# Kernel optimization log

Hardware: AMD Instinct MI355X
Metric: run time of the kernel (lower is better)

The kernel has to match this reference:

```python
import jax, jax.numpy as jnp
import numpy as np

N = 8192       # nodes
E = 262144     # edges (avg degree 32)
F_IN, H, L = 512, 256, 64


def setup_inputs() -> dict:
    key = jax.random.key(0)
    ks = jax.random.split(key, 8)
    features = jax.random.normal(ks[0], (N, F_IN), dtype=jnp.float32)
    src = jax.random.randint(ks[1], (E,), 0, N)
    dst = jax.random.randint(ks[2], (E,), 0, N)
    # nn.Linear weights are [out_feats, in_feats]; scale ~ kaiming-ish small init
    W1 = jax.random.normal(ks[3], (H, F_IN), dtype=jnp.float32) * (1.0 / np.sqrt(F_IN))
    b1 = jnp.zeros((H,), dtype=jnp.float32)
    W2 = jax.random.normal(ks[4], (L, H), dtype=jnp.float32) * (1.0 / np.sqrt(H))
    b2 = jnp.zeros((L,), dtype=jnp.float32)
    W3 = jax.random.normal(ks[5], (L, H), dtype=jnp.float32) * (1.0 / np.sqrt(H))
    b3 = jnp.zeros((L,), dtype=jnp.float32)
    return {"features": features, "src": src, "dst": dst,
            "W1": W1, "b1": b1, "W2": W2, "b2": b2, "W3": W3, "b3": b3}


def _gcn_agg(h, src, dst):
    # DGL copy_src + sum: gather source node features along edges, scatter-sum to dst
    return jax.ops.segment_sum(h[src], dst, num_segments=N)  # [N, d]


def reference(features, src, dst, W1, b1, W2, b2, W3, b3):
    # GCN layer 1: aggregate then linear + relu  (dropout=0 -> identity)
    agg1 = _gcn_agg(features, src, dst)                 # [N, F_IN]
    hidden = jax.nn.relu(agg1 @ W1.T + b1)              # [N, H]
    # GCN layers 2 & 3 share the aggregated hidden (linear activation)
    agg2 = _gcn_agg(hidden, src, dst)                   # [N, H]
    mu = agg2 @ W2.T + b2                               # [N, L]
    logvar = agg2 @ W3.T + b3                           # [N, L]
    # eval-mode reparameterize: z = mu
    z = mu
    # inner-product decoder with sigmoid
    adj = jax.nn.sigmoid(z @ z.T)                       # [N, N]
    return adj, mu, logvar
```

## Files before the change

kernel.cpp:

```cpp
#include <hip/hip_runtime.h>
#include <hip/hip_bf16.h>
#include <type_traits>

#define N_NODES 8192
#define N_EDGES 262144

typedef __attribute__((ext_vector_type(8))) short short8v;
typedef __attribute__((ext_vector_type(4))) float float4v;

static __device__ __forceinline__ unsigned short f2bf(float f) {
    unsigned u = __float_as_uint(f);
    unsigned r = (u + 0x7FFF + ((u >> 16) & 1)) >> 16;
    return (unsigned short)r;
}
static __device__ __forceinline__ float bf2f(unsigned short h) {
    return __uint_as_float(((unsigned)h) << 16);
}


__global__ __launch_bounds__(256) void hist_kernel(const int* __restrict__ dst, int* __restrict__ deg) {
    int e = blockIdx.x * 256 + threadIdx.x;
    if (e < N_EDGES) atomicAdd(&deg[dst[e]], 1);
}

__global__ __launch_bounds__(1024) void scan_kernel(const int* __restrict__ deg, int* __restrict__ offs) {
    __shared__ int sums[1024];
    int t = threadIdx.x;
    int v[8];
    int s = 0;
#pragma unroll
    for (int i = 0; i < 8; i++) { v[i] = deg[t * 8 + i]; s += v[i]; }
    sums[t] = s;
    __syncthreads();
    for (int off = 1; off < 1024; off <<= 1) {
        int x = (t >= off) ? sums[t - off] : 0;
        __syncthreads();
        sums[t] += x;
        __syncthreads();
    }
    int ex = (t == 0) ? 0 : sums[t - 1];
#pragma unroll
    for (int i = 0; i < 8; i++) { offs[t * 8 + i] = ex; ex += v[i]; }
    if (t == 1023) offs[N_NODES] = ex;
}

__global__ __launch_bounds__(256) void scatter_kernel(const int* __restrict__ src, const int* __restrict__ dst,
                                                      const int* __restrict__ offs, int* __restrict__ cur,
                                                      int* __restrict__ csr) {
    int e = blockIdx.x * 256 + threadIdx.x;
    if (e < N_EDGES) {
        int d = dst[e];
        int p = atomicAdd(&cur[d], 1);
        csr[offs[d] + p] = src[e];
    }
}

__global__ __launch_bounds__(256) void concat_w_kernel(const float* __restrict__ W2, const float* __restrict__ W3,
                                                       float* __restrict__ W23) {
    int i = blockIdx.x * 256 + threadIdx.x;
    if (i < 16384) W23[i] = W2[i];
    else if (i < 32768) W23[i] = W3[i - 16384];
}


template <int BM, int BN, int BK, int TM, int TN, bool BF16_OUT>
__global__ __launch_bounds__(256) void gemm_nt(const float* __restrict__ A, const float* __restrict__ B,
                                               void* __restrict__ Cv, int M, int N, int K) {
    __shared__ float As[BK][BM + 4];
    __shared__ float Bs[BK][BN + 4];
    const int tid = threadIdx.x;
    const int tc = tid % (BN / TN);
    const int tr = tid / (BN / TN);
    const int m0 = blockIdx.x * BM;
    const int n0 = blockIdx.y * BN;
    float acc[TM][TN] = {};
    for (int k0 = 0; k0 < K; k0 += BK) {
        constexpr int A_LOADS = BM * BK / (256 * 4);
#pragma unroll
        for (int i = 0; i < A_LOADS; i++) {
            int idx = (tid + i * 256) * 4;
            int am = idx / BK, ak = idx % BK;
            float4 v = *(const float4*)&A[(size_t)(m0 + am) * K + k0 + ak];
            As[ak + 0][am] = v.x; As[ak + 1][am] = v.y; As[ak + 2][am] = v.z; As[ak + 3][am] = v.w;
        }
        constexpr int B_LOADS = BN * BK / (256 * 4);
#pragma unroll
        for (int i = 0; i < B_LOADS; i++) {
            int idx = (tid + i * 256) * 4;
            int bn = idx / BK, bk = idx % BK;
            float4 v = *(const float4*)&B[(size_t)(n0 + bn) * K + k0 + bk];
            Bs[bk + 0][bn] = v.x; Bs[bk + 1][bn] = v.y; Bs[bk + 2][bn] = v.z; Bs[bk + 3][bn] = v.w;
        }
        __syncthreads();
#pragma unroll
        for (int k = 0; k < BK; k++) {
            float a[TM], b[TN];
#pragma unroll
            for (int i = 0; i < TM; i += 4) *(float4*)&a[i] = *(const float4*)&As[k][tr * TM + i];
#pragma unroll
            for (int j = 0; j < TN; j += 4) *(float4*)&b[j] = *(const float4*)&Bs[k][tc * TN + j];
#pragma unroll
            for (int i = 0; i < TM; i++)
#pragma unroll
                for (int j = 0; j < TN; j++) acc[i][j] = fmaf(a[i], b[j], acc[i][j]);
        }
        __syncthreads();
    }
#pragma unroll
    for (int i = 0; i < TM; i++) {
        size_t row = (size_t)(m0 + tr * TM + i) * N + n0 + tc * TN;
        if constexpr (BF16_OUT) {
            unsigned short* C = (unsigned short*)Cv;
#pragma unroll
            for (int j = 0; j < TN; j += 4) {
                ushort4 v;
                v.x = f2bf(acc[i][j]); v.y = f2bf(acc[i][j + 1]);
                v.z = f2bf(acc[i][j + 2]); v.w = f2bf(acc[i][j + 3]);
                *(ushort4*)&C[row + j] = v;
            }
        } else {
            float* C = (float*)Cv;
#pragma unroll
            for (int j = 0; j < TN; j += 4) {
                float4 v = {acc[i][j], acc[i][j + 1], acc[i][j + 2], acc[i][j + 3]};
                *(float4*)&C[row + j] = v;
            }
        }
    }
}


__global__ __launch_bounds__(256) void agg_relu_kernel(const unsigned short* __restrict__ Yb,
                                                       const int* __restrict__ offs,
                                                       const int* __restrict__ csr, const float* __restrict__ bias,
                                                       float* __restrict__ out) {
    int node = blockIdx.x * 4 + (threadIdx.x >> 6);
    int lane = threadIdx.x & 63;
    int s = offs[node], e = offs[node + 1];
    float4 acc = {0.f, 0.f, 0.f, 0.f};
    for (int i = s; i < e; i++) {
        int u = csr[i];
        ushort4 v = *(const ushort4*)&Yb[(size_t)u * 256 + lane * 4];
        acc.x += bf2f(v.x); acc.y += bf2f(v.y); acc.z += bf2f(v.z); acc.w += bf2f(v.w);
    }
    float4 b = *(const float4*)&bias[lane * 4];
    acc.x = fmaxf(acc.x + b.x, 0.f);
    acc.y = fmaxf(acc.y + b.y, 0.f);
    acc.z = fmaxf(acc.z + b.z, 0.f);
    acc.w = fmaxf(acc.w + b.w, 0.f);
    *(float4*)&out[(size_t)node * 256 + lane * 4] = acc;
}


__global__ __launch_bounds__(256) void agg_split_kernel(const unsigned short* __restrict__ Zb,
                                                        const int* __restrict__ offs,
                                                        const int* __restrict__ csr, const float* __restrict__ b2,
                                                        const float* __restrict__ b3, float* __restrict__ mu,
                                                        float* __restrict__ lv, unsigned short* __restrict__ zb) {
    int node = blockIdx.x * 4 + (threadIdx.x >> 6);
    int lane = threadIdx.x & 63;
    int s = offs[node], e = offs[node + 1];
    float2 acc = {0.f, 0.f};
    for (int i = s; i < e; i++) {
        int u = csr[i];
        ushort2 v = *(const ushort2*)&Zb[(size_t)u * 128 + lane * 2];
        acc.x += bf2f(v.x); acc.y += bf2f(v.y);
    }
    int col = lane * 2;
    if (col < 64) {
        acc.x += b2[col]; acc.y += b2[col + 1];
        *(float2*)&mu[(size_t)node * 64 + col] = acc;
        ushort2 q = {f2bf(acc.x), f2bf(acc.y)};
        *(ushort2*)&zb[(size_t)node * 64 + col] = q;
    } else {
        col -= 64;
        acc.x += b3[col]; acc.y += b3[col + 1];
        *(float2*)&lv[(size_t)node * 64 + col] = acc;
    }
}


__global__ __launch_bounds__(256) void adj_mfma_kernel(const unsigned short* __restrict__ zb,
                                                       float* __restrict__ out) {
    const int tid = threadIdx.x;
    const int lane = tid & 63;
    const int wid = tid >> 6;
    const int waveM = wid >> 1, waveN = wid & 1;
    const int m_base = blockIdx.x * 128 + waveM * 64;
    const int n_base = blockIdx.y * 128 + waveN * 64;
    const int r = lane & 15;
    const int q = lane >> 4;

    short8v a[4][2], b[4][2];
#pragma unroll
    for (int i = 0; i < 4; i++)
#pragma unroll
        for (int s = 0; s < 2; s++) {
            a[i][s] = *(const short8v*)&zb[(size_t)(m_base + i * 16 + r) * 64 + s * 32 + q * 8];
            b[i][s] = *(const short8v*)&zb[(size_t)(n_base + i * 16 + r) * 64 + s * 32 + q * 8];
        }

    float4v acc[4][4] = {};
#pragma unroll
    for (int s = 0; s < 2; s++)
#pragma unroll
        for (int i = 0; i < 4; i++)
#pragma unroll
            for (int j = 0; j < 4; j++)
                acc[i][j] = __builtin_amdgcn_mfma_f32_16x16x32_bf16(a[i][s], b[j][s], acc[i][j], 0, 0, 0);

#pragma unroll
    for (int i = 0; i < 4; i++)
#pragma unroll
        for (int j = 0; j < 4; j++) {
            int col = n_base + j * 16 + r;
#pragma unroll
            for (int t = 0; t < 4; t++) {
                int row = m_base + i * 16 + q * 4 + t;
                float v = 1.0f / (1.0f + __expf(-acc[i][j][t]));
                out[(size_t)row * N_NODES + col] = v;
            }
        }
}


extern "C" void kernel_launch(void* const* d_in, const int* in_sizes, int n_in,
                              void* d_out, int out_size, void* d_ws, size_t ws_size,
                              hipStream_t stream) {
    const float* X   = (const float*)d_in[0];
    const int*   src = (const int*)d_in[1];
    const int*   dst = (const int*)d_in[2];
    const float* W1  = (const float*)d_in[3];
    const float* b1  = (const float*)d_in[4];
    const float* W2  = (const float*)d_in[5];
    const float* b2  = (const float*)d_in[6];
    const float* W3  = (const float*)d_in[7];
    const float* b3  = (const float*)d_in[8];

    float* out    = (float*)d_out;
    float* adj    = out;
    float* mu_out = out + (size_t)N_NODES * N_NODES;
    float* lv_out = mu_out + (size_t)N_NODES * 64;

    char* ws = (char*)d_ws;
    int* deg             = (int*)(ws + 0);
    int* cur             = (int*)(ws + 32768);
    int* offs            = (int*)(ws + 65536);
    int* csr             = (int*)(ws + 98816);
    float* W23           = (float*)(ws + 1179648);
    unsigned short* Y1b  = (unsigned short*)(ws + 1310720);
    float* hidden        = (float*)(ws + 5505024);
    unsigned short* Zb   = (unsigned short*)(ws + 13893632);
    unsigned short* zb   = (unsigned short*)(ws + 15990784);

    hipMemsetAsync(deg, 0, 2 * N_NODES * sizeof(int), stream);
    hist_kernel<<<N_EDGES / 256, 256, 0, stream>>>(dst, deg);
    scan_kernel<<<1, 1024, 0, stream>>>(deg, offs);
    scatter_kernel<<<N_EDGES / 256, 256, 0, stream>>>(src, dst, offs, cur, csr);
    concat_w_kernel<<<128, 256, 0, stream>>>(W2, W3, W23);

    gemm_nt<64, 64, 16, 4, 4, true><<<dim3(128, 4), 256, 0, stream>>>(X, W1, Y1b, 8192, 256, 512);
    agg_relu_kernel<<<N_NODES / 4, 256, 0, stream>>>(Y1b, offs, csr, b1, hidden);
    gemm_nt<64, 64, 16, 4, 4, true><<<dim3(128, 2), 256, 0, stream>>>(hidden, W23, Zb, 8192, 128, 256);
    agg_split_kernel<<<N_NODES / 4, 256, 0, stream>>>(Zb, offs, csr, b2, b3, mu_out, lv_out, zb);
    adj_mfma_kernel<<<dim3(64, 64), 256, 0, stream>>>(zb, adj);
}
```

Baseline: 419.9 us.

## Switch dense GEMMs to bf16 MFMA with pre-cast inputs and bf16 hidden

```diff
diff --git a/kernel.cpp b/kernel.cpp
--- a/kernel.cpp
+++ b/kernel.cpp
@@ -1,6 +1,5 @@
 #include <hip/hip_runtime.h>
 #include <hip/hip_bf16.h>
-#include <type_traits>
 
 #define N_NODES 8192
 #define N_EDGES 262144
@@ -55,100 +54,97 @@
     }
 }
 
-__global__ __launch_bounds__(256) void concat_w_kernel(const float* __restrict__ W2, const float* __restrict__ W3,
-                                                       float* __restrict__ W23) {
-    int i = blockIdx.x * 256 + threadIdx.x;
-    if (i < 16384) W23[i] = W2[i];
-    else if (i < 32768) W23[i] = W3[i - 16384];
-}
-
-
-template <int BM, int BN, int BK, int TM, int TN, bool BF16_OUT>
-__global__ __launch_bounds__(256) void gemm_nt(const float* __restrict__ A, const float* __restrict__ B,
-                                               void* __restrict__ Cv, int M, int N, int K) {
-    __shared__ float As[BK][BM + 4];
-    __shared__ float Bs[BK][BN + 4];
+
+__global__ __launch_bounds__(256) void prep_cast_kernel(const float* __restrict__ X, const float* __restrict__ W1,
+                                                        const float* __restrict__ W2, const float* __restrict__ W3,
+                                                        unsigned short* __restrict__ Xb,
+                                                        unsigned short* __restrict__ W1b,
+                                                        unsigned short* __restrict__ W23b) {
+    int i4 = (blockIdx.x * 256 + threadIdx.x) * 4;
+    const float* srcp;
+    unsigned short* dstp;
+    int off;
+    if (i4 < 4194304)      { srcp = X;  dstp = Xb;           off = i4; }
+    else if (i4 < 4325376) { srcp = W1; dstp = W1b;          off = i4 - 4194304; }
+    else if (i4 < 4341760) { srcp = W2; dstp = W23b;         off = i4 - 4325376; }
+    else                   { srcp = W3; dstp = W23b + 16384; off = i4 - 4341760; }
+    float4 v = *(const float4*)&srcp[off];
+    ushort4 o = {f2bf(v.x), f2bf(v.y), f2bf(v.z), f2bf(v.w)};
+    *(ushort4*)&dstp[off] = o;
+}
+
+
+template <int MI, int NJ, int WN>
+__global__ __launch_bounds__(256) void gemm_nt_mfma(const unsigned short* __restrict__ A,
+                                                    const unsigned short* __restrict__ B,
+                                                    unsigned short* __restrict__ C,
+                                                    int N, int K) {
+    constexpr int MW = 4 / WN;
     const int tid = threadIdx.x;
-    const int tc = tid % (BN / TN);
-    const int tr = tid / (BN / TN);
-    const int m0 = blockIdx.x * BM;
-    const int n0 = blockIdx.y * BN;
-    float acc[TM][TN] = {};
-    for (int k0 = 0; k0 < K; k0 += BK) {
-        constexpr int A_LOADS = BM * BK / (256 * 4);
-#pragma unroll
-        for (int i = 0; i < A_LOADS; i++) {
-            int idx = (tid + i * 256) * 4;
-            int am = idx / BK, ak = idx % BK;
-            float4 v = *(const float4*)&A[(size_t)(m0 + am) * K + k0 + ak];
-            As[ak + 0][am] = v.x; As[ak + 1][am] = v.y; As[ak + 2][am] = v.z; As[ak + 3][am] = v.w;
-        }
-        constexpr int B_LOADS = BN * BK / (256 * 4);
-#pragma unroll
-        for (int i = 0; i < B_LOADS; i++) {
-            int idx = (tid + i * 256) * 4;
-            int bn = idx / BK, bk = idx % BK;
-            float4 v = *(const float4*)&B[(size_t)(n0 + bn) * K + k0 + bk];
-            Bs[bk + 0][bn] = v.x; Bs[bk + 1][bn] = v.y; Bs[bk + 2][bn] = v.z; Bs[bk + 3][bn] = v.w;
-        }
-        __syncthreads();
-#pragma unroll
-        for (int k = 0; k < BK; k++) {
-            float a[TM], b[TN];
-#pragma unroll
-            for (int i = 0; i < TM; i += 4) *(float4*)&a[i] = *(const float4*)&As[k][tr * TM + i];
-#pragma unroll
-            for (int j = 0; j < TN; j += 4) *(float4*)&b[j] = *(const float4*)&Bs[k][tc * TN + j];
-#pragma unroll
-            for (int i = 0; i < TM; i++)
-#pragma unroll
-                for (int j = 0; j < TN; j++) acc[i][j] = fmaf(a[i], b[j], acc[i][j]);
-        }
-        __syncthreads();
-    }
-#pragma unroll
-    for (int i = 0; i < TM; i++) {
-        size_t row = (size_t)(m0 + tr * TM + i) * N + n0 + tc * TN;
-        if constexpr (BF16_OUT) {
-            unsigned short* C = (unsigned short*)Cv;
-#pragma unroll
-            for (int j = 0; j < TN; j += 4) {
-                ushort4 v;
-                v.x = f2bf(acc[i][j]); v.y = f2bf(acc[i][j + 1]);
-                v.z = f2bf(acc[i][j + 2]); v.w = f2bf(acc[i][j + 3]);
-                *(ushort4*)&C[row + j] = v;
-            }
-        } else {
-            float* C = (float*)Cv;
-#pragma unroll
-            for (int j = 0; j < TN; j += 4) {
-                float4 v = {acc[i][j], acc[i][j + 1], acc[i][j + 2], acc[i][j + 3]};
-                *(float4*)&C[row + j] = v;
+    const int lane = tid & 63;
+    const int w = tid >> 6;
+    const int r = lane & 15, q = lane >> 4;
+    const int m0 = blockIdx.x * (MI * 16 * MW) + (w / WN) * (MI * 16);
+    const int n0 = blockIdx.y * (NJ * 16 * WN) + (w % WN) * (NJ * 16);
+    float4v acc[MI][NJ] = {};
+    for (int k = 0; k < K; k += 32) {
+        short8v a[MI], b[NJ];
+#pragma unroll
+        for (int i = 0; i < MI; i++)
+            a[i] = *(const short8v*)&A[(size_t)(m0 + i * 16 + r) * K + k + q * 8];
+#pragma unroll
+        for (int j = 0; j < NJ; j++)
+            b[j] = *(const short8v*)&B[(size_t)(n0 + j * 16 + r) * K + k + q * 8];
+#pragma unroll
+        for (int i = 0; i < MI; i++)
+#pragma unroll
+            for (int j = 0; j < NJ; j++)
+                acc[i][j] = __builtin_amdgcn_mfma_f32_16x16x32_bf16(a[i], b[j], acc[i][j], 0, 0, 0);
+    }
+#pragma unroll
+    for (int i = 0; i < MI; i++)
+#pragma unroll
+        for (int j = 0; j < NJ; j++) {
+            int col = n0 + j * 16 + r;
+#pragma unroll
+            for (int t = 0; t < 4; t++) {
+                int row = m0 + i * 16 + q * 4 + t;
+                C[(size_t)row * N + col] = f2bf(acc[i][j][t]);
             }
         }
-    }
 }
 
 
 __global__ __launch_bounds__(256) void agg_relu_kernel(const unsigned short* __restrict__ Yb,
                                                        const int* __restrict__ offs,
                                                        const int* __restrict__ csr, const float* __restrict__ bias,
-                                                       float* __restrict__ out) {
+                                                       unsigned short* __restrict__ out) {
     int node = blockIdx.x * 4 + (threadIdx.x >> 6);
     int lane = threadIdx.x & 63;
     int s = offs[node], e = offs[node + 1];
     float4 acc = {0.f, 0.f, 0.f, 0.f};
-    for (int i = s; i < e; i++) {
+    int i = s;
+    for (; i + 1 < e; i += 2) {
+        int u0 = csr[i], u1 = csr[i + 1];
+        ushort4 v0 = *(const ushort4*)&Yb[(size_t)u0 * 256 + lane * 4];
+        ushort4 v1 = *(const ushort4*)&Yb[(size_t)u1 * 256 + lane * 4];
+        acc.x += bf2f(v0.x) + bf2f(v1.x);
+        acc.y += bf2f(v0.y) + bf2f(v1.y);
+        acc.z += bf2f(v0.z) + bf2f(v1.z);
+        acc.w += bf2f(v0.w) + bf2f(v1.w);
+    }
+    if (i < e) {
         int u = csr[i];
         ushort4 v = *(const ushort4*)&Yb[(size_t)u * 256 + lane * 4];
         acc.x += bf2f(v.x); acc.y += bf2f(v.y); acc.z += bf2f(v.z); acc.w += bf2f(v.w);
     }
     float4 b = *(const float4*)&bias[lane * 4];
-    acc.x = fmaxf(acc.x + b.x, 0.f);
-    acc.y = fmaxf(acc.y + b.y, 0.f);
-    acc.z = fmaxf(acc.z + b.z, 0.f);
-    acc.w = fmaxf(acc.w + b.w, 0.f);
-    *(float4*)&out[(size_t)node * 256 + lane * 4] = acc;
+    ushort4 o;
+    o.x = f2bf(fmaxf(acc.x + b.x, 0.f));
+    o.y = f2bf(fmaxf(acc.y + b.y, 0.f));
+    o.z = f2bf(fmaxf(acc.z + b.z, 0.f));
+    o.w = f2bf(fmaxf(acc.w + b.w, 0.f));
+    *(ushort4*)&out[(size_t)node * 256 + lane * 4] = o;
 }
 
 
@@ -161,7 +157,15 @@
     int lane = threadIdx.x & 63;
     int s = offs[node], e = offs[node + 1];
     float2 acc = {0.f, 0.f};
-    for (int i = s; i < e; i++) {
+    int i = s;
+    for (; i + 1 < e; i += 2) {
+        int u0 = csr[i], u1 = csr[i + 1];
+        ushort2 v0 = *(const ushort2*)&Zb[(size_t)u0 * 128 + lane * 2];
+        ushort2 v1 = *(const ushort2*)&Zb[(size_t)u1 * 128 + lane * 2];
+        acc.x += bf2f(v0.x) + bf2f(v1.x);
+        acc.y += bf2f(v0.y) + bf2f(v1.y);
+    }
+    if (i < e) {
         int u = csr[i];
         ushort2 v = *(const ushort2*)&Zb[(size_t)u * 128 + lane * 2];
         acc.x += bf2f(v.x); acc.y += bf2f(v.y);
@@ -243,25 +247,33 @@
     float* lv_out = mu_out + (size_t)N_NODES * 64;
 
     char* ws = (char*)d_ws;
-    int* deg             = (int*)(ws + 0);
-    int* cur             = (int*)(ws + 32768);
-    int* offs            = (int*)(ws + 65536);
-    int* csr             = (int*)(ws + 98816);
-    float* W23           = (float*)(ws + 1179648);
-    unsigned short* Y1b  = (unsigned short*)(ws + 1310720);
-    float* hidden        = (float*)(ws + 5505024);
-    unsigned short* Zb   = (unsigned short*)(ws + 13893632);
-    unsigned short* zb   = (unsigned short*)(ws + 15990784);
+    size_t off = 0;
+    auto alloc = [&](size_t bytes) -> void* {
+        void* p = ws + off;
+        off += (bytes + 1023) & ~(size_t)1023;
+        return p;
+    };
+    int* deg            = (int*)alloc(N_NODES * 4);
+    int* cur            = (int*)alloc(N_NODES * 4);
+    int* offs           = (int*)alloc((N_NODES + 1) * 4);
+    int* csr            = (int*)alloc(N_EDGES * 4);
+    unsigned short* Xb  = (unsigned short*)alloc((size_t)N_NODES * 512 * 2);
+    unsigned short* W1b = (unsigned short*)alloc(256 * 512 * 2);
+    unsigned short* W23b= (unsigned short*)alloc(128 * 256 * 2);
+    unsigned short* Y1b = (unsigned short*)alloc((size_t)N_NODES * 256 * 2);
+    unsigned short* Hb  = (unsigned short*)alloc((size_t)N_NODES * 256 * 2);
+    unsigned short* Zb  = (unsigned short*)alloc((size_t)N_NODES * 128 * 2);
+    unsigned short* zb  = (unsigned short*)alloc((size_t)N_NODES * 64 * 2);
 
     hipMemsetAsync(deg, 0, 2 * N_NODES * sizeof(int), stream);
     hist_kernel<<<N_EDGES / 256, 256, 0, stream>>>(dst, deg);
     scan_kernel<<<1, 1024, 0, stream>>>(deg, offs);
     scatter_kernel<<<N_EDGES / 256, 256, 0, stream>>>(src, dst, offs, cur, csr);
-    concat_w_kernel<<<128, 256, 0, stream>>>(W2, W3, W23);
-
-    gemm_nt<64, 64, 16, 4, 4, true><<<dim3(128, 4), 256, 0, stream>>>(X, W1, Y1b, 8192, 256, 512);
-    agg_relu_kernel<<<N_NODES / 4, 256, 0, stream>>>(Y1b, offs, csr, b1, hidden);
-    gemm_nt<64, 64, 16, 4, 4, true><<<dim3(128, 2), 256, 0, stream>>>(hidden, W23, Zb, 8192, 128, 256);
+    prep_cast_kernel<<<4256, 256, 0, stream>>>(X, W1, W2, W3, Xb, W1b, W23b);
+
+    gemm_nt_mfma<4, 2, 4><<<dim3(128, 2), 256, 0, stream>>>(Xb, W1b, Y1b, 256, 512);
+    agg_relu_kernel<<<N_NODES / 4, 256, 0, stream>>>(Y1b, offs, csr, b1, Hb);
+    gemm_nt_mfma<4, 1, 4><<<dim3(128, 2), 256, 0, stream>>>(Hb, W23b, Zb, 128, 256);
     agg_split_kernel<<<N_NODES / 4, 256, 0, stream>>>(Zb, offs, csr, b2, b3, mu_out, lv_out, zb);
     adj_mfma_kernel<<<dim3(64, 64), 256, 0, stream>>>(zb, adj);
 }
```

After: 383.5 us. 8.7% less time.
